# Optimization experiments

Hardware: AMD Instinct MI355X
Metric: run time of the kernel (lower is better)

The kernel has to match this reference:

```python
import jax, jax.numpy as jnp
import numpy as np

C = 16        # channel_n
HID = 128     # hidden width of 1x1 MLP
FIRE_RATE = 0.5
STEP_SIZE = 1.0
ALIVE_THRESH = 0.1
B, H, W = 16, 256, 256


def _perceive_kernel():
    # identity + Sobel filters, angle = 0.0 so cos=1, sin=0
    ident = np.outer([0.0, 1.0, 0.0], [0.0, 1.0, 0.0]).astype(np.float32)
    dxk = (np.outer([1.0, 2.0, 1.0], [-1.0, 0.0, 1.0]) / 8.0).astype(np.float32)
    dyk = dxk.T
    k3 = np.stack([ident, dxk, dyk], axis=-1)  # [3,3,3]
    # TF depthwise layout: out channel index = c*3 + k  -> tile over channels
    rhs = np.tile(k3, (1, 1, C)).reshape(3, 3, 1, 3 * C)  # HWIO, groups=C
    return jnp.asarray(rhs)


def _get_living_mask(x):
    alpha = x[:, :, :, 3:4]
    pooled = jax.lax.reduce_window(alpha, -jnp.inf, jax.lax.max,
                                   (1, 3, 3, 1), (1, 1, 1, 1), 'SAME')
    return pooled > ALIVE_THRESH


def _perceive(x):
    rhs = _perceive_kernel()
    return jax.lax.conv_general_dilated(
        x, rhs, window_strides=(1, 1), padding='SAME',
        dimension_numbers=('NHWC', 'HWIO', 'NHWC'),
        feature_group_count=C)  # [B,H,W,3C]


def setup_inputs() -> dict:
    key = jax.random.key(0)
    kx, kw1, kb1, ku = jax.random.split(key, 4)
    x = jax.random.normal(kx, (B, H, W, C), dtype=jnp.float32)
    # dmodel params: Conv2D(128,1,relu) then Conv2D(16,1,zeros init); use
    # random values for a meaningful numeric baseline
    W1 = jax.random.normal(kw1, (3 * C, HID), dtype=jnp.float32) * 0.1
    b1 = jax.random.normal(kb1, (HID,), dtype=jnp.float32) * 0.01
    W2 = jax.random.normal(jax.random.fold_in(key, 7), (HID, C), dtype=jnp.float32) * 0.1
    b2 = jnp.zeros((C,), dtype=jnp.float32)
    rand_u = jax.random.uniform(ku, (B, H, W, 1), dtype=jnp.float32)
    return {"x": x, "W1": W1, "b1": b1, "W2": W2, "b2": b2, "rand_u": rand_u}


def reference(x, W1, b1, W2, b2, rand_u):
    pre_life_mask = _get_living_mask(x)
    y = _perceive(x)                                         # [B,H,W,48]
    h = jax.nn.relu(jnp.einsum('bhwc,cd->bhwd', y, W1) + b1)  # [B,H,W,128]
    dx = (jnp.einsum('bhwd,dc->bhwc', h, W2) + b2) * STEP_SIZE
    update_mask = (rand_u <= FIRE_RATE).astype(x.dtype)
    x = x + dx * update_mask
    post_life_mask = _get_living_mask(x)
    life_mask = (pre_life_mask & post_life_mask).astype(x.dtype)
    return x * life_mask
```

## Files before the change

### kernel.cpp

```cpp
#include <hip/hip_runtime.h>


#define NC 16
#define NHID 128
#define NPIX (16 * 256 * 256)
#define MG 0.04f
#define MAXFIX 65536

typedef __attribute__((ext_vector_type(8))) short s8b;
typedef __attribute__((ext_vector_type(4))) float f4;

__device__ __forceinline__ unsigned short f2bf(float f) {
    union { float f; unsigned int u; } v; v.f = f;
    unsigned int r = (v.u + 0x7FFFu + ((v.u >> 16) & 1u)) >> 16;
    return (unsigned short)r;
}
__device__ __forceinline__ unsigned int pack2(float a, float b) {
    return (unsigned int)f2bf(a) | ((unsigned int)f2bf(b) << 16);
}

__global__ __launch_bounds__(256) void ca_prep(
    const float* __restrict__ W1, const float* __restrict__ b1,
    const float* __restrict__ W2, uint4* __restrict__ w1p, uint4* __restrict__ w2p)
{
    const int tid = threadIdx.x;
    if (blockIdx.x == 0) {
        for (int idx = tid; idx < 1024; idx += 256) {
            const int fid = idx >> 6, lane = idx & 63;
            const int k0 = fid >> 3, mt = fid & 7;
            const int q = lane >> 4, i = lane & 15;
            unsigned int u[4];
            #pragma unroll
            for (int jp = 0; jp < 4; ++jp) {
                int k = k0 * 32 + q * 8 + jp * 2;
                float v0 = (k < 48) ? W1[k * 128 + mt * 16 + i] : ((k == 48) ? b1[mt * 16 + i] : 0.f);
                k++;
                float v1 = (k < 48) ? W1[k * 128 + mt * 16 + i] : ((k == 48) ? b1[mt * 16 + i] : 0.f);
                u[jp] = pack2(v0, v1);
            }
            w1p[idx] = make_uint4(u[0], u[1], u[2], u[3]);
        }
    } else {
        for (int idx = tid; idx < 256; idx += 256) {
            const int k2 = idx >> 6, lane = idx & 63;
            const int q = lane >> 4, i = lane & 15;
            unsigned int u[4];
            #pragma unroll
            for (int jp = 0; jp < 4; ++jp) {
                const int k = k2 * 32 + q * 8 + jp * 2;
                u[jp] = pack2(W2[k * 16 + i], W2[(k + 1) * 16 + i]);
            }
            w2p[idx] = make_uint4(u[0], u[1], u[2], u[3]);
        }
    }
}

__global__ __launch_bounds__(256, 2) void ca_update(
    const float* __restrict__ x, const float* __restrict__ b2,
    const float* __restrict__ rand_u, const uint4* __restrict__ w1p,
    const uint4* __restrict__ w2p, float* __restrict__ out,
    float* __restrict__ ws_alpha, unsigned char* __restrict__ ws_pre,
    unsigned int* __restrict__ fix_cnt, unsigned int* __restrict__ fix_list)
{
    __shared__ __align__(16) float xt[18 * 18 * 20];
    __shared__ __align__(16) unsigned short yfs[4 * 2 * 528];
    __shared__ __align__(16) unsigned short hbs[4 * 16 * 136];
    __shared__ float lsr[256];

    const int tid  = threadIdx.x;
    const int lane = tid & 63;
    const int li   = lane & 15;
    const int lq   = lane >> 4;
    const int wv   = tid >> 6;
    const int tx   = tid & 15, ty = tid >> 4;
    const int w0 = blockIdx.x * 16, h0 = blockIdx.y * 16, bb = blockIdx.z;

    s8b w1f[2][8], w2f[4];
    const s8b* w1s = (const s8b*)w1p;
    const s8b* w2s = (const s8b*)w2p;
    #pragma unroll
    for (int k0 = 0; k0 < 2; ++k0)
        #pragma unroll
        for (int mt = 0; mt < 8; ++mt)
            w1f[k0][mt] = w1s[(k0 * 8 + mt) * 64 + lane];
    #pragma unroll
    for (int k2 = 0; k2 < 4; ++k2) w2f[k2] = w2s[k2 * 64 + lane];
    float b2v[4];
    #pragma unroll
    for (int r = 0; r < 4; ++r) b2v[r] = b2[lq * 4 + r];

    for (int i = tid; i < 324; i += 256) {
        const int ly = i / 18, lx = i - ly * 18;
        const int gh = h0 + ly - 1, gw = w0 + lx - 1;
        float4 v0, v1, v2, v3;
        if (gh >= 0 && gh < 256 && gw >= 0 && gw < 256) {
            const float4* p = (const float4*)(x + (((size_t)bb * 256 + gh) * 256 + gw) * NC);
            v0 = p[0]; v1 = p[1]; v2 = p[2]; v3 = p[3];
        } else {
            v0 = v1 = v2 = v3 = make_float4(0.f, 0.f, 0.f, 0.f);
        }
        float4* t = (float4*)(xt + i * 20);
        t[0] = v0; t[1] = v1; t[2] = v2; t[3] = v3;
    }
    const size_t gpix = ((size_t)bb * 256 + h0 + ty) * 256 + (w0 + tx);
    lsr[tid] = rand_u[gpix];
    __syncthreads();

    const int o_mm = ((ty + 0) * 18 + tx + 0) * 20, o_m0 = ((ty + 0) * 18 + tx + 1) * 20, o_mp = ((ty + 0) * 18 + tx + 2) * 20;
    const int o_0m = ((ty + 1) * 18 + tx + 0) * 20, o_cc = ((ty + 1) * 18 + tx + 1) * 20, o_0p = ((ty + 1) * 18 + tx + 2) * 20;
    const int o_pm = ((ty + 2) * 18 + tx + 0) * 20, o_p0 = ((ty + 2) * 18 + tx + 1) * 20, o_pp = ((ty + 2) * 18 + tx + 2) * 20;

    float am = xt[o_mm + 3];
    am = fmaxf(am, xt[o_m0 + 3]); am = fmaxf(am, xt[o_mp + 3]);
    am = fmaxf(am, xt[o_0m + 3]); am = fmaxf(am, xt[o_cc + 3]); am = fmaxf(am, xt[o_0p + 3]);
    am = fmaxf(am, xt[o_pm + 3]); am = fmaxf(am, xt[o_p0 + 3]); am = fmaxf(am, xt[o_pp + 3]);
    ws_pre[gpix] = (am > 0.1f) ? (unsigned char)1 : (unsigned char)0;

    unsigned int yu[24];
    #pragma unroll
    for (int cq = 0; cq < 4; ++cq) {
        const int co = cq * 4;
        float4 vmm = *(const float4*)(xt + o_mm + co); const float* pmm = (const float*)&vmm;
        float4 vm0 = *(const float4*)(xt + o_m0 + co); const float* pm0 = (const float*)&vm0;
        float4 vmp = *(const float4*)(xt + o_mp + co); const float* pmp = (const float*)&vmp;
        float4 v0m = *(const float4*)(xt + o_0m + co); const float* p0m = (const float*)&v0m;
        float4 vcc = *(const float4*)(xt + o_cc + co); const float* pcc = (const float*)&vcc;
        float4 v0p = *(const float4*)(xt + o_0p + co); const float* p0p = (const float*)&v0p;
        float4 vpm = *(const float4*)(xt + o_pm + co); const float* ppm = (const float*)&vpm;
        float4 vp0 = *(const float4*)(xt + o_p0 + co); const float* pp0 = (const float*)&vp0;
        float4 vpp = *(const float4*)(xt + o_pp + co); const float* ppp = (const float*)&vpp;
        float yl[12];
        #pragma unroll
        for (int cc = 0; cc < 4; ++cc) {
            const float xmm = pmm[cc], xm0 = pm0[cc], xmp = pmp[cc];
            const float x0m = p0m[cc], xcc = pcc[cc], x0p = p0p[cc];
            const float xpm = ppm[cc], xp0 = pp0[cc], xpp = ppp[cc];
            yl[cc * 3 + 0] = xcc;
            yl[cc * 3 + 1] = ((xmp - xmm) + 2.f * (x0p - x0m) + (xpp - xpm)) * 0.125f;
            yl[cc * 3 + 2] = ((xpm - xmm) + 2.f * (xp0 - xm0) + (xpp - xmp)) * 0.125f;
        }
        #pragma unroll
        for (int m2 = 0; m2 < 6; ++m2) yu[cq * 6 + m2] = pack2(yl[2 * m2], yl[2 * m2 + 1]);
    }

    unsigned short* yfw = yfs + wv * (2 * 528);
    unsigned short* hbw = hbs + wv * (16 * 136);

    for (int s = 0; s < 4; ++s) {
        const int t = wv * 4 + s;
        if ((ty & 3) == s) {
            #pragma unroll
            for (int q = 0; q < 4; ++q)
                *(uint4*)(yfw + (q * 16 + tx) * 8) = make_uint4(yu[q * 4], yu[q * 4 + 1], yu[q * 4 + 2], yu[q * 4 + 3]);
            *(uint4*)(yfw + 528 + (0 * 16 + tx) * 8) = make_uint4(yu[16], yu[17], yu[18], yu[19]);
            *(uint4*)(yfw + 528 + (1 * 16 + tx) * 8) = make_uint4(yu[20], yu[21], yu[22], yu[23]);
            *(uint4*)(yfw + 528 + (2 * 16 + tx) * 8) = make_uint4(0x3F80u, 0u, 0u, 0u);
            *(uint4*)(yfw + 528 + (3 * 16 + tx) * 8) = make_uint4(0u, 0u, 0u, 0u);
        }
        const s8b ya0 = *(const s8b*)(yfw + lane * 8);
        const s8b ya1 = *(const s8b*)(yfw + 528 + lane * 8);
        f4 acc1[8];
        #pragma unroll
        for (int mt = 0; mt < 8; ++mt) { f4 z = {0.f, 0.f, 0.f, 0.f}; acc1[mt] = z; }
        #pragma unroll
        for (int mt = 0; mt < 8; ++mt)
            acc1[mt] = __builtin_amdgcn_mfma_f32_16x16x32_bf16(w1f[0][mt], ya0, acc1[mt], 0, 0, 0);
        #pragma unroll
        for (int mt = 0; mt < 8; ++mt)
            acc1[mt] = __builtin_amdgcn_mfma_f32_16x16x32_bf16(w1f[1][mt], ya1, acc1[mt], 0, 0, 0);
        #pragma unroll
        for (int mt = 0; mt < 8; ++mt) {
            const float hh0 = fmaxf(acc1[mt][0], 0.f), hh1 = fmaxf(acc1[mt][1], 0.f);
            const float hh2 = fmaxf(acc1[mt][2], 0.f), hh3 = fmaxf(acc1[mt][3], 0.f);
            *(uint2*)(hbw + li * 136 + mt * 16 + lq * 4) = make_uint2(pack2(hh0, hh1), pack2(hh2, hh3));
        }
        f4 acc2 = {0.f, 0.f, 0.f, 0.f};
        #pragma unroll
        for (int k2 = 0; k2 < 4; ++k2) {
            const s8b hf = *(const s8b*)(hbw + li * 136 + k2 * 32 + lq * 8);
            acc2 = __builtin_amdgcn_mfma_f32_16x16x32_bf16(w2f[k2], hf, acc2, 0, 0, 0);
        }
        const float um = (lsr[t * 16 + li] <= 0.5f) ? 1.f : 0.f;
        const float4 xc = *(const float4*)(xt + ((t + 1) * 18 + li + 1) * 20 + lq * 4);
        float4 nx;
        nx.x = fmaf(acc2[0] + b2v[0], um, xc.x);
        nx.y = fmaf(acc2[1] + b2v[1], um, xc.y);
        nx.z = fmaf(acc2[2] + b2v[2], um, xc.z);
        nx.w = fmaf(acc2[3] + b2v[3], um, xc.w);
        const size_t gp = ((size_t)bb * 256 + h0 + t) * 256 + (w0 + li);
        ((float4*)out)[gp * 4 + lq] = nx;
        if (lq == 0) {
            ws_alpha[gp] = nx.w;
            if (um != 0.f && fabsf(nx.w - 0.1f) <= MG) {
                unsigned int idx = atomicAdd(fix_cnt, 1u);
                if (idx < MAXFIX) fix_list[idx] = (unsigned int)gp;
            }
        }
    }
}

__global__ __launch_bounds__(64) void ca_fix(
    const float* __restrict__ x, const float* __restrict__ W1,
    const float* __restrict__ b1, const float* __restrict__ W2,
    const float* __restrict__ b2,
    const unsigned int* __restrict__ fix_cnt, const unsigned int* __restrict__ fix_list,
    float* __restrict__ ws_alpha)
{
    __shared__ float ysh[48];
    const int lane = threadIdx.x;
    unsigned int n = *fix_cnt;
    if (n > MAXFIX) n = MAXFIX;
    for (unsigned int e = blockIdx.x; e < n; e += gridDim.x) {
        const unsigned int pix = fix_list[e];
        const int bb = pix >> 16, h = (pix >> 8) & 255, w = pix & 255;
        if (lane < 48) {
            const int c = lane / 3, j = lane - c * 3;
            float v = 0.f;
            #pragma unroll
            for (int dy = 0; dy < 3; ++dy) {
                #pragma unroll
                for (int dxx = 0; dxx < 3; ++dxx) {
                    const int hh = h + dy - 1, ww = w + dxx - 1;
                    if (hh < 0 || hh >= 256 || ww < 0 || ww >= 256) continue;
                    const float f = x[(((size_t)bb * 256 + hh) * 256 + ww) * 16 + c];
                    float wgt;
                    if (j == 0) wgt = (dy == 1 && dxx == 1) ? 1.f : 0.f;
                    else if (j == 1) wgt = ((dy == 1) ? 2.f : 1.f) * (float)(dxx - 1) * 0.125f;
                    else wgt = ((dxx == 1) ? 2.f : 1.f) * (float)(dy - 1) * 0.125f;
                    v = fmaf(f, wgt, v);
                }
            }
            ysh[lane] = v;
        }
        __syncthreads();
        float dot = 0.f;
        #pragma unroll
        for (int t = 0; t < 2; ++t) {
            const int d = t * 64 + lane;
            float a = b1[d];
            #pragma unroll
            for (int k = 0; k < 48; ++k)
                a = fmaf(ysh[k], W1[k * 128 + d], a);
            dot = fmaf(fmaxf(a, 0.f), W2[d * 16 + 3], dot);
        }
        #pragma unroll
        for (int off = 32; off > 0; off >>= 1)
            dot += __shfl_down(dot, off, 64);
        if (lane == 0)
            ws_alpha[pix] = x[(size_t)pix * 16 + 3] + dot + b2[3];
        __syncthreads();
    }
}

__global__ __launch_bounds__(256) void ca_mask(
    const float* __restrict__ alpha, const unsigned char* __restrict__ pre,
    float* __restrict__ out)
{
    __shared__ float at[18 * 20];
    const int tid = threadIdx.x;
    const int w0 = blockIdx.x * 16, h0 = blockIdx.y * 16, bb = blockIdx.z;
    for (int i = tid; i < 324; i += 256) {
        const int ly = i / 18, lx = i - ly * 18;
        const int gh = h0 + ly - 1, gw = w0 + lx - 1;
        float v = 0.f;
        if (gh >= 0 && gh < 256 && gw >= 0 && gw < 256)
            v = alpha[((size_t)bb * 256 + gh) * 256 + gw];
        at[ly * 20 + lx] = v;
    }
    __syncthreads();
    const int txx = tid & 15, tyy = tid >> 4;
    float m = at[tyy * 20 + txx];
    m = fmaxf(m, at[tyy * 20 + txx + 1]); m = fmaxf(m, at[tyy * 20 + txx + 2]);
    m = fmaxf(m, at[(tyy + 1) * 20 + txx]); m = fmaxf(m, at[(tyy + 1) * 20 + txx + 1]); m = fmaxf(m, at[(tyy + 1) * 20 + txx + 2]);
    m = fmaxf(m, at[(tyy + 2) * 20 + txx]); m = fmaxf(m, at[(tyy + 2) * 20 + txx + 1]); m = fmaxf(m, at[(tyy + 2) * 20 + txx + 2]);
    const size_t gp = ((size_t)bb * 256 + h0 + tyy) * 256 + (w0 + txx);
    const bool alive = (m > 0.1f) && pre[gp];
    if (!alive) {
        float4* po = (float4*)(out + gp * 16);
        const float4 z = make_float4(0.f, 0.f, 0.f, 0.f);
        po[0] = z; po[1] = z; po[2] = z; po[3] = z;
    }
}

extern "C" void kernel_launch(void* const* d_in, const int* in_sizes, int n_in,
                              void* d_out, int out_size, void* d_ws, size_t ws_size,
                              hipStream_t stream) {
    (void)in_sizes; (void)n_in; (void)out_size; (void)ws_size;
    const float* x  = (const float*)d_in[0];
    const float* W1 = (const float*)d_in[1];
    const float* b1 = (const float*)d_in[2];
    const float* W2 = (const float*)d_in[3];
    const float* b2 = (const float*)d_in[4];
    const float* ru = (const float*)d_in[5];
    float* out = (float*)d_out;

    char* ws = (char*)d_ws;
    float* ws_alpha       = (float*)ws;
    unsigned char* ws_pre = (unsigned char*)(ws + (size_t)NPIX * 4);
    uint4* w1p            = (uint4*)(ws + (size_t)NPIX * 5);
    uint4* w2p            = w1p + 1024;
    unsigned int* fix_cnt = (unsigned int*)(ws + (size_t)NPIX * 5 + 20480);
    unsigned int* fix_list= fix_cnt + 4;

    hipMemsetAsync(fix_cnt, 0, sizeof(unsigned int), stream);
    ca_prep<<<2, 256, 0, stream>>>(W1, b1, W2, w1p, w2p);
    dim3 g(16, 16, 16);
    ca_update<<<g, 256, 0, stream>>>(x, b2, ru, w1p, w2p, out, ws_alpha, ws_pre, fix_cnt, fix_list);
    ca_fix<<<4096, 64, 0, stream>>>(x, W1, b1, W2, b2, fix_cnt, fix_list, ws_alpha);
    ca_mask<<<g, 256, 0, stream>>>(ws_alpha, ws_pre, out);
}
```

Baseline: 333.4 us.

## Stage weights in reused LDS and pass hidden activations via shuffles for occupancy

Weight fragments for both MFMA layers now live in shared memory, reusing the input-tile buffer after the Sobel stage, instead of being held in registers for the whole kernel. The hidden-layer staging buffer is removed, and ReLU outputs are moved into B-operand layout with lane shuffles. The second GEMM is split into two accumulators. Launch bounds go from 2 to 4 waves per SIMD to raise occupancy. In exchange, the kernel adds extra LDS reads of weights on every pass, adds many shuffles, and reads the center x from global memory again instead of from LDS.

New measurement: 352.3 us. +5.7%, slower.

```diff
diff --git a/kernel.cpp b/kernel.cpp
--- a/kernel.cpp
+++ b/kernel.cpp
@@ -55,16 +55,15 @@
     }
 }
 
-__global__ __launch_bounds__(256, 2) void ca_update(
+__global__ __launch_bounds__(256, 4) void ca_update(
     const float* __restrict__ x, const float* __restrict__ b2,
     const float* __restrict__ rand_u, const uint4* __restrict__ w1p,
     const uint4* __restrict__ w2p, float* __restrict__ out,
     float* __restrict__ ws_alpha, unsigned char* __restrict__ ws_pre,
     unsigned int* __restrict__ fix_cnt, unsigned int* __restrict__ fix_list)
 {
-    __shared__ __align__(16) float xt[18 * 18 * 20];
+    __shared__ __align__(16) float xw[18 * 18 * 20];
     __shared__ __align__(16) unsigned short yfs[4 * 2 * 528];
-    __shared__ __align__(16) unsigned short hbs[4 * 16 * 136];
     __shared__ float lsr[256];
 
     const int tid  = threadIdx.x;
@@ -75,16 +74,6 @@
     const int tx   = tid & 15, ty = tid >> 4;
     const int w0 = blockIdx.x * 16, h0 = blockIdx.y * 16, bb = blockIdx.z;
 
-    s8b w1f[2][8], w2f[4];
-    const s8b* w1s = (const s8b*)w1p;
-    const s8b* w2s = (const s8b*)w2p;
-    #pragma unroll
-    for (int k0 = 0; k0 < 2; ++k0)
-        #pragma unroll
-        for (int mt = 0; mt < 8; ++mt)
-            w1f[k0][mt] = w1s[(k0 * 8 + mt) * 64 + lane];
-    #pragma unroll
-    for (int k2 = 0; k2 < 4; ++k2) w2f[k2] = w2s[k2 * 64 + lane];
     float b2v[4];
     #pragma unroll
     for (int r = 0; r < 4; ++r) b2v[r] = b2[lq * 4 + r];
@@ -99,7 +88,7 @@
         } else {
             v0 = v1 = v2 = v3 = make_float4(0.f, 0.f, 0.f, 0.f);
         }
-        float4* t = (float4*)(xt + i * 20);
+        float4* t = (float4*)(xw + i * 20);
         t[0] = v0; t[1] = v1; t[2] = v2; t[3] = v3;
     }
     const size_t gpix = ((size_t)bb * 256 + h0 + ty) * 256 + (w0 + tx);
@@ -110,25 +99,25 @@
     const int o_0m = ((ty + 1) * 18 + tx + 0) * 20, o_cc = ((ty + 1) * 18 + tx + 1) * 20, o_0p = ((ty + 1) * 18 + tx + 2) * 20;
     const int o_pm = ((ty + 2) * 18 + tx + 0) * 20, o_p0 = ((ty + 2) * 18 + tx + 1) * 20, o_pp = ((ty + 2) * 18 + tx + 2) * 20;
 
-    float am = xt[o_mm + 3];
-    am = fmaxf(am, xt[o_m0 + 3]); am = fmaxf(am, xt[o_mp + 3]);
-    am = fmaxf(am, xt[o_0m + 3]); am = fmaxf(am, xt[o_cc + 3]); am = fmaxf(am, xt[o_0p + 3]);
-    am = fmaxf(am, xt[o_pm + 3]); am = fmaxf(am, xt[o_p0 + 3]); am = fmaxf(am, xt[o_pp + 3]);
+    float am = xw[o_mm + 3];
+    am = fmaxf(am, xw[o_m0 + 3]); am = fmaxf(am, xw[o_mp + 3]);
+    am = fmaxf(am, xw[o_0m + 3]); am = fmaxf(am, xw[o_cc + 3]); am = fmaxf(am, xw[o_0p + 3]);
+    am = fmaxf(am, xw[o_pm + 3]); am = fmaxf(am, xw[o_p0 + 3]); am = fmaxf(am, xw[o_pp + 3]);
     ws_pre[gpix] = (am > 0.1f) ? (unsigned char)1 : (unsigned char)0;
 
     unsigned int yu[24];
     #pragma unroll
     for (int cq = 0; cq < 4; ++cq) {
         const int co = cq * 4;
-        float4 vmm = *(const float4*)(xt + o_mm + co); const float* pmm = (const float*)&vmm;
-        float4 vm0 = *(const float4*)(xt + o_m0 + co); const float* pm0 = (const float*)&vm0;
-        float4 vmp = *(const float4*)(xt + o_mp + co); const float* pmp = (const float*)&vmp;
-        float4 v0m = *(const float4*)(xt + o_0m + co); const float* p0m = (const float*)&v0m;
-        float4 vcc = *(const float4*)(xt + o_cc + co); const float* pcc = (const float*)&vcc;
-        float4 v0p = *(const float4*)(xt + o_0p + co); const float* p0p = (const float*)&v0p;
-        float4 vpm = *(const float4*)(xt + o_pm + co); const float* ppm = (const float*)&vpm;
-        float4 vp0 = *(const float4*)(xt + o_p0 + co); const float* pp0 = (const float*)&vp0;
-        float4 vpp = *(const float4*)(xt + o_pp + co); const float* ppp = (const float*)&vpp;
+        float4 vmm = *(const float4*)(xw + o_mm + co); const float* pmm = (const float*)&vmm;
+        float4 vm0 = *(const float4*)(xw + o_m0 + co); const float* pm0 = (const float*)&vm0;
+        float4 vmp = *(const float4*)(xw + o_mp + co); const float* pmp = (const float*)&vmp;
+        float4 v0m = *(const float4*)(xw + o_0m + co); const float* p0m = (const float*)&v0m;
+        float4 vcc = *(const float4*)(xw + o_cc + co); const float* pcc = (const float*)&vcc;
+        float4 v0p = *(const float4*)(xw + o_0p + co); const float* p0p = (const float*)&v0p;
+        float4 vpm = *(const float4*)(xw + o_pm + co); const float* ppm = (const float*)&vpm;
+        float4 vp0 = *(const float4*)(xw + o_p0 + co); const float* pp0 = (const float*)&vp0;
+        float4 vpp = *(const float4*)(xw + o_pp + co); const float* ppp = (const float*)&vpp;
         float yl[12];
         #pragma unroll
         for (int cc = 0; cc < 4; ++cc) {
@@ -142,9 +131,20 @@
         #pragma unroll
         for (int m2 = 0; m2 < 6; ++m2) yu[cq * 6 + m2] = pack2(yl[2 * m2], yl[2 * m2 + 1]);
     }
-
+    __syncthreads();
+
+    for (int i = tid; i < 1280; i += 256) {
+        const uint4 v = (i < 1024) ? w1p[i] : w2p[i - 1024];
+        ((uint4*)xw)[i] = v;
+    }
+    __syncthreads();
+
+    const unsigned short* wl = (const unsigned short*)xw;
     unsigned short* yfw = yfs + wv * (2 * 528);
-    unsigned short* hbw = hbs + wv * (16 * 136);
+
+    const int srcA = li + (lq & 1) * 32;
+    const int srcB = srcA + 16;
+    const bool hiq = (lq >= 2);
 
     for (int s = 0; s < 4; ++s) {
         const int t = wv * 4 + s;
@@ -159,35 +159,53 @@
         }
         const s8b ya0 = *(const s8b*)(yfw + lane * 8);
         const s8b ya1 = *(const s8b*)(yfw + 528 + lane * 8);
+
         f4 acc1[8];
         #pragma unroll
         for (int mt = 0; mt < 8; ++mt) { f4 z = {0.f, 0.f, 0.f, 0.f}; acc1[mt] = z; }
         #pragma unroll
-        for (int mt = 0; mt < 8; ++mt)
-            acc1[mt] = __builtin_amdgcn_mfma_f32_16x16x32_bf16(w1f[0][mt], ya0, acc1[mt], 0, 0, 0);
-        #pragma unroll
-        for (int mt = 0; mt < 8; ++mt)
-            acc1[mt] = __builtin_amdgcn_mfma_f32_16x16x32_bf16(w1f[1][mt], ya1, acc1[mt], 0, 0, 0);
-        #pragma unroll
         for (int mt = 0; mt < 8; ++mt) {
-            const float hh0 = fmaxf(acc1[mt][0], 0.f), hh1 = fmaxf(acc1[mt][1], 0.f);
-            const float hh2 = fmaxf(acc1[mt][2], 0.f), hh3 = fmaxf(acc1[mt][3], 0.f);
-            *(uint2*)(hbw + li * 136 + mt * 16 + lq * 4) = make_uint2(pack2(hh0, hh1), pack2(hh2, hh3));
-        }
-        f4 acc2 = {0.f, 0.f, 0.f, 0.f};
+            const s8b wf = *(const s8b*)(wl + mt * 512 + lane * 8);
+            acc1[mt] = __builtin_amdgcn_mfma_f32_16x16x32_bf16(wf, ya0, acc1[mt], 0, 0, 0);
+        }
+        #pragma unroll
+        for (int mt = 0; mt < 8; ++mt) {
+            const s8b wf = *(const s8b*)(wl + (8 + mt) * 512 + lane * 8);
+            acc1[mt] = __builtin_amdgcn_mfma_f32_16x16x32_bf16(wf, ya1, acc1[mt], 0, 0, 0);
+        }
+
+        f4 acc2[2];
+        { f4 z = {0.f, 0.f, 0.f, 0.f}; acc2[0] = z; acc2[1] = z; }
         #pragma unroll
         for (int k2 = 0; k2 < 4; ++k2) {
-            const s8b hf = *(const s8b*)(hbw + li * 136 + k2 * 32 + lq * 8);
-            acc2 = __builtin_amdgcn_mfma_f32_16x16x32_bf16(w2f[k2], hf, acc2, 0, 0, 0);
-        }
+            const f4 aE = acc1[2 * k2], aO = acc1[2 * k2 + 1];
+            const unsigned int e0 = pack2(fmaxf(aE[0], 0.f), fmaxf(aE[1], 0.f));
+            const unsigned int e1 = pack2(fmaxf(aE[2], 0.f), fmaxf(aE[3], 0.f));
+            const unsigned int o0 = pack2(fmaxf(aO[0], 0.f), fmaxf(aO[1], 0.f));
+            const unsigned int o1 = pack2(fmaxf(aO[2], 0.f), fmaxf(aO[3], 0.f));
+            const unsigned int vE0A = (unsigned int)__shfl((int)e0, srcA, 64);
+            const unsigned int vE1A = (unsigned int)__shfl((int)e1, srcA, 64);
+            const unsigned int vO0A = (unsigned int)__shfl((int)o0, srcA, 64);
+            const unsigned int vO1A = (unsigned int)__shfl((int)o1, srcA, 64);
+            const unsigned int vE0B = (unsigned int)__shfl((int)e0, srcB, 64);
+            const unsigned int vE1B = (unsigned int)__shfl((int)e1, srcB, 64);
+            const unsigned int vO0B = (unsigned int)__shfl((int)o0, srcB, 64);
+            const unsigned int vO1B = (unsigned int)__shfl((int)o1, srcB, 64);
+            union { uint4 u; s8b v; } hb;
+            hb.u = make_uint4(hiq ? vO0A : vE0A, hiq ? vO1A : vE1A,
+                              hiq ? vO0B : vE0B, hiq ? vO1B : vE1B);
+            const s8b w2fr = *(const s8b*)(wl + 8192 + k2 * 512 + lane * 8);
+            acc2[k2 >> 1] = __builtin_amdgcn_mfma_f32_16x16x32_bf16(w2fr, hb.v, acc2[k2 >> 1], 0, 0, 0);
+        }
+
         const float um = (lsr[t * 16 + li] <= 0.5f) ? 1.f : 0.f;
-        const float4 xc = *(const float4*)(xt + ((t + 1) * 18 + li + 1) * 20 + lq * 4);
+        const size_t gp = ((size_t)bb * 256 + h0 + t) * 256 + (w0 + li);
+        const float4 xc = ((const float4*)x)[gp * 4 + lq];
         float4 nx;
-        nx.x = fmaf(acc2[0] + b2v[0], um, xc.x);
-        nx.y = fmaf(acc2[1] + b2v[1], um, xc.y);
-        nx.z = fmaf(acc2[2] + b2v[2], um, xc.z);
-        nx.w = fmaf(acc2[3] + b2v[3], um, xc.w);
-        const size_t gp = ((size_t)bb * 256 + h0 + t) * 256 + (w0 + li);
+        nx.x = fmaf(acc2[0][0] + acc2[1][0] + b2v[0], um, xc.x);
+        nx.y = fmaf(acc2[0][1] + acc2[1][1] + b2v[1], um, xc.y);
+        nx.z = fmaf(acc2[0][2] + acc2[1][2] + b2v[2], um, xc.z);
+        nx.w = fmaf(acc2[0][3] + acc2[1][3] + b2v[3], um, xc.w);
         ((float4*)out)[gp * 4 + lq] = nx;
         if (lq == 0) {
             ws_alpha[gp] = nx.w;
```
